# Kernel optimization log

Hardware: AMD Instinct MI355X
Metric: run time of the kernel (lower is better)

## Reference

```python
import jax, jax.numpy as jnp
import numpy as np

IMG = 1024.0
MAXD = 8.0
EPS = 1e-6
ENC_HEADS = 12
DEC_HEADS = 16


def _ln(x, w, b):
    m = jnp.mean(x, -1, keepdims=True)
    v = jnp.mean((x - m) ** 2, -1, keepdims=True)
    return (x - m) / jnp.sqrt(v + EPS) * w + b


def _attn(x, qkv_w, qkv_b, pr_w, pr_b, nh, key_mask):
    B, L, D = x.shape
    hd = D // nh
    qkv = (x @ qkv_w + qkv_b).reshape(B, L, 3, nh, hd).transpose(2, 0, 3, 1, 4)
    q, k, v = qkv[0], qkv[1], qkv[2]  # [B, nh, L, hd]
    s = jnp.einsum('bhqd,bhkd->bhqk', q, k) * (hd ** -0.5)
    if key_mask is not None:
        # restrict attention to visible tokens; identical math to per-sample gather+encode
        s = jnp.where(key_mask[:, None, None, :], s, -1e9)
    a = jax.nn.softmax(s, -1)
    o = jnp.einsum('bhqk,bhkd->bhqd', a, v).transpose(0, 2, 1, 3).reshape(B, L, D)
    return o @ pr_w + pr_b


def _block(x, i, ln1w, ln1b, qkvw, qkvb, prw, prb, ln2w, ln2b, f1w, f1b, f2w, f2b, nh, key_mask):
    x = x + _attn(_ln(x, ln1w[i], ln1b[i]), qkvw[i], qkvb[i], prw[i], prb[i], nh, key_mask)
    h = jax.nn.gelu(_ln(x, ln2w[i], ln2b[i]) @ f1w[i] + f1b[i], approximate=False)
    return x + h @ f2w[i] + f2b[i]


def _pos(coords, depths, w1, b1, w2, b2):
    x1, x2, y1, y2 = coords[..., 0], coords[..., 1], coords[..., 2], coords[..., 3]
    f = jnp.stack([(x1 + x2) / 2.0 / IMG, (y1 + y2) / 2.0 / IMG,
                   (x2 - x1) / IMG, (y2 - y1) / IMG, depths / MAXD], -1)
    return jax.nn.gelu(f @ w1 + b1, approximate=False) @ w2 + b2


def _forward(patches, coords, depths, pe_w, pe_b, pos1_w, pos1_b, pos2_w, pos2_b,
             e_ln1_w, e_ln1_b, e_qkv_w, e_qkv_b, e_pr_w, e_pr_b, e_ln2_w, e_ln2_b,
             e_f1_w, e_f1_b, e_f2_w, e_f2_b, enorm_w, enorm_b,
             de_w, de_b, mask_token, dpos1_w, dpos1_b, dpos2_w, dpos2_b,
             d_ln1_w, d_ln1_b, d_qkv_w, d_qkv_b, d_pr_w, d_pr_b, d_ln2_w, d_ln2_b,
             d_f1_w, d_f1_b, d_f2_w, d_f2_b, dnorm_w, dnorm_b,
             hi_w, hi_b, hn_w, hn_b, mask):
    B, L = mask.shape
    x = patches.reshape(B, L, -1) @ pe_w + pe_b + _pos(coords, depths, pos1_w, pos1_b, pos2_w, pos2_b)
    visible = (mask == 0)
    h = x
    for i in range(e_qkv_w.shape[0]):
        h = _block(h, i, e_ln1_w, e_ln1_b, e_qkv_w, e_qkv_b, e_pr_w, e_pr_b,
                   e_ln2_w, e_ln2_b, e_f1_w, e_f1_b, e_f2_w, e_f2_b, ENC_HEADS, visible)
    encoded = jnp.where(visible[..., None], _ln(h, enorm_w, enorm_b), 0.0)
    xd = encoded @ de_w + de_b
    xd = jnp.where((mask != 0)[..., None], mask_token, xd)
    xd = xd + _pos(coords, depths, dpos1_w, dpos1_b, dpos2_w, dpos2_b)
    for i in range(d_qkv_w.shape[0]):
        xd = _block(xd, i, d_ln1_w, d_ln1_b, d_qkv_w, d_qkv_b, d_pr_w, d_pr_b,
                    d_ln2_w, d_ln2_b, d_f1_w, d_f1_b, d_f2_w, d_f2_b, DEC_HEADS, None)
    xd = _ln(xd, dnorm_w, dnorm_b)
    return (xd @ hi_w + hi_b, xd @ hn_w + hn_b)


def setup_inputs() -> dict:
    key = jax.random.key(0)
    ks = iter(jax.random.split(key, 80))
    def nrm(shape, std=0.02):
        return jax.random.normal(next(ks), shape, jnp.float32) * std
    B, L, P, C = 4, 512, 32, 1
    D, DD = 768, 512
    ED, DDEP = 12, 8
    pd = C * P * P
    inp = {}
    inp['patches'] = jax.random.normal(next(ks), (B, L, C, P, P), jnp.float32)
    inp['coords'] = jax.random.uniform(next(ks), (B, L, 4), jnp.float32)
    inp['depths'] = jax.random.uniform(next(ks), (B, L), jnp.float32)
    inp['mask'] = jax.random.randint(next(ks), (B, L), 0, 2, jnp.int32)
    inp['pe_w'] = nrm((pd, D)); inp['pe_b'] = jnp.zeros((D,))
    inp['pos1_w'] = nrm((5, D // 2)); inp['pos1_b'] = jnp.zeros((D // 2,))
    inp['pos2_w'] = nrm((D // 2, D)); inp['pos2_b'] = jnp.zeros((D,))
    inp['e_ln1_w'] = jnp.ones((ED, D)); inp['e_ln1_b'] = jnp.zeros((ED, D))
    inp['e_qkv_w'] = nrm((ED, D, 3 * D)); inp['e_qkv_b'] = jnp.zeros((ED, 3 * D))
    inp['e_pr_w'] = nrm((ED, D, D)); inp['e_pr_b'] = jnp.zeros((ED, D))
    inp['e_ln2_w'] = jnp.ones((ED, D)); inp['e_ln2_b'] = jnp.zeros((ED, D))
    inp['e_f1_w'] = nrm((ED, D, 4 * D)); inp['e_f1_b'] = jnp.zeros((ED, 4 * D))
    inp['e_f2_w'] = nrm((ED, 4 * D, D)); inp['e_f2_b'] = jnp.zeros((ED, D))
    inp['enorm_w'] = jnp.ones((D,)); inp['enorm_b'] = jnp.zeros((D,))
    inp['de_w'] = nrm((D, DD)); inp['de_b'] = jnp.zeros((DD,))
    inp['mask_token'] = nrm((DD,))
    inp['dpos1_w'] = nrm((5, DD // 2)); inp['dpos1_b'] = jnp.zeros((DD // 2,))
    inp['dpos2_w'] = nrm((DD // 2, DD)); inp['dpos2_b'] = jnp.zeros((DD,))
    inp['d_ln1_w'] = jnp.ones((DDEP, DD)); inp['d_ln1_b'] = jnp.zeros((DDEP, DD))
    inp['d_qkv_w'] = nrm((DDEP, DD, 3 * DD)); inp['d_qkv_b'] = jnp.zeros((DDEP, 3 * DD))
    inp['d_pr_w'] = nrm((DDEP, DD, DD)); inp['d_pr_b'] = jnp.zeros((DDEP, DD))
    inp['d_ln2_w'] = jnp.ones((DDEP, DD)); inp['d_ln2_b'] = jnp.zeros((DDEP, DD))
    inp['d_f1_w'] = nrm((DDEP, DD, 4 * DD)); inp['d_f1_b'] = jnp.zeros((DDEP, 4 * DD))
    inp['d_f2_w'] = nrm((DDEP, 4 * DD, DD)); inp['d_f2_b'] = jnp.zeros((DDEP, DD))
    inp['dnorm_w'] = jnp.ones((DD,)); inp['dnorm_b'] = jnp.zeros((DD,))
    inp['hi_w'] = nrm((DD, pd)); inp['hi_b'] = jnp.zeros((pd,))
    inp['hn_w'] = nrm((DD, pd)); inp['hn_b'] = jnp.zeros((pd,))
    return inp


def reference(patches, coords, depths, pe_w, pe_b, pos1_w, pos1_b, pos2_w, pos2_b,
              e_ln1_w, e_ln1_b, e_qkv_w, e_qkv_b, e_pr_w, e_pr_b, e_ln2_w, e_ln2_b,
              e_f1_w, e_f1_b, e_f2_w, e_f2_b, enorm_w, enorm_b,
              de_w, de_b, mask_token, dpos1_w, dpos1_b, dpos2_w, dpos2_b,
              d_ln1_w, d_ln1_b, d_qkv_w, d_qkv_b, d_pr_w, d_pr_b, d_ln2_w, d_ln2_b,
              d_f1_w, d_f1_b, d_f2_w, d_f2_b, dnorm_w, dnorm_b,
              hi_w, hi_b, hn_w, hn_b, mask):
    return _forward(patches, coords, depths, pe_w, pe_b, pos1_w, pos1_b, pos2_w, pos2_b,
                    e_ln1_w, e_ln1_b, e_qkv_w, e_qkv_b, e_pr_w, e_pr_b, e_ln2_w, e_ln2_b,
                    e_f1_w, e_f1_b, e_f2_w, e_f2_b, enorm_w, enorm_b,
                    de_w, de_b, mask_token, dpos1_w, dpos1_b, dpos2_w, dpos2_b,
                    d_ln1_w, d_ln1_b, d_qkv_w, d_qkv_b, d_pr_w, d_pr_b, d_ln2_w, d_ln2_b,
                    d_f1_w, d_f1_b, d_f2_w, d_f2_b, dnorm_w, dnorm_b,
                    hi_w, hi_b, hn_w, hn_b, mask)
```

## Files before the change

kernel.cpp:

```cpp
#include <hip/hip_runtime.h>
#include <hip/hip_bf16.h>

using bf16 = __hip_bfloat16;
typedef __bf16 bf16x8 __attribute__((ext_vector_type(8)));
typedef float f32x4 __attribute__((ext_vector_type(4)));

__device__ __forceinline__ float gelu_exact(float x) {
    return 0.5f * x * (1.0f + erff(x * 0.70710678118654752440f));
}

#define GLD_LDS16(g, l) __builtin_amdgcn_global_load_lds( \
    (__attribute__((address_space(1))) void*)(g),          \
    (__attribute__((address_space(3))) void*)(l), 16, 0, 0)

template<int BM,int BN,int WM,int WN,int FM,int FN,int OUT_BF16,int HAS_BIAS,int HAS_RES,int DO_GELU>
__global__ __launch_bounds__(256, 4) void gemm_bt(
    const bf16* __restrict__ A, long lda,
    const bf16* __restrict__ Bt, long ldb,
    void* __restrict__ Cv, long ldc,
    const float* __restrict__ bias, const float* __restrict__ Res,
    int K, float alpha)
{
    static_assert(WM * WN == 4 && BM == WM * FM * 16 && BN == WN * FN * 16, "cfg");
    __shared__ alignas(16) unsigned short As[2][BM * 32];
    __shared__ alignas(16) unsigned short Bs[2][BN * 32];

    const int nwg = gridDim.x * gridDim.y;
    const int orig = blockIdx.y * gridDim.x + blockIdx.x;
    const int q = nwg >> 3, r = nwg & 7;
    const int xcd = orig & 7, seq = orig >> 3;
    const int wg = (xcd < r ? xcd * (q + 1) : r * (q + 1) + (xcd - r) * q) + seq;
    const int bn0 = (wg % gridDim.x) * BN;
    const int bm0 = (wg / gridDim.x) * BM;

    const int tid = threadIdx.x;
    const int wave = tid >> 6, lane = tid & 63;
    const int wm = (wave / WN) * (FM * 16);
    const int wn = (wave % WN) * (FN * 16);

    f32x4 acc[FM][FN] = {};

    constexpr int CA = BM / 16, CT = (BM + BN) / 16;
    constexpr int LPT = CT / 4;
    static_assert(CT % 4 == 0 && (LPT == 2 || LPT == 3), "stage cfg");
    const int lrow = lane >> 2;
    const int lcol = (((lane & 3) ^ ((lrow >> 1) & 3)) * 8);
    const int nk = K >> 5;

    const int fr = lane & 15;
    const int kg = lane >> 4;
    const int kswz = (kg ^ ((fr >> 1) & 3)) * 8;

    auto stage = [&](int buf, int kt) {
        const int k0 = kt * 32;
        for (int c = wave; c < CT; c += 4) {
            if (c < CA) {
                const bf16* src = A + (long)(bm0 + c * 16 + lrow) * lda + k0 + lcol;
                GLD_LDS16(src, &As[buf][c * 512]);
            } else {
                const int c2 = c - CA;
                const bf16* src = Bt + (long)(bn0 + c2 * 16 + lrow) * ldb + k0 + lcol;
                GLD_LDS16(src, &Bs[buf][c2 * 512]);
            }
        }
    };

    stage(0, 0);
    if (nk > 1) stage(1, 1);
    int cur = 0;
    for (int kt = 0; kt < nk; ++kt) {
        if (kt + 1 < nk) {
            if constexpr (LPT == 3) asm volatile("s_waitcnt vmcnt(3)" ::: "memory");
            else                    asm volatile("s_waitcnt vmcnt(2)" ::: "memory");
        } else {
            asm volatile("s_waitcnt vmcnt(0)" ::: "memory");
        }
        __builtin_amdgcn_s_barrier();
        __builtin_amdgcn_sched_barrier(0);

        bf16x8 af[FM], bfv[FN];
        #pragma unroll
        for (int m = 0; m < FM; ++m)
            af[m] = *(const bf16x8*)&As[cur][(wm + m * 16 + fr) * 32 + kswz];
        #pragma unroll
        for (int n = 0; n < FN; ++n)
            bfv[n] = *(const bf16x8*)&Bs[cur][(wn + n * 16 + fr) * 32 + kswz];
        #pragma unroll
        for (int m = 0; m < FM; ++m)
            #pragma unroll
            for (int n = 0; n < FN; ++n)
                acc[m][n] = __builtin_amdgcn_mfma_f32_16x16x32_bf16(af[m], bfv[n], acc[m][n], 0, 0, 0);

        __builtin_amdgcn_sched_barrier(0);
        asm volatile("s_waitcnt lgkmcnt(0)" ::: "memory");
        __builtin_amdgcn_s_barrier();
        if (kt + 2 < nk) stage(cur, kt + 2);
        cur ^= 1;
    }

    const int r0 = (lane >> 4) * 4;
    #pragma unroll
    for (int m = 0; m < FM; ++m) {
        const int rowb = bm0 + wm + m * 16 + r0;
        #pragma unroll
        for (int n = 0; n < FN; ++n) {
            const int col = bn0 + wn + n * 16 + fr;
            #pragma unroll
            for (int j = 0; j < 4; ++j) {
                float v = acc[m][n][j] * alpha;
                if (HAS_BIAS) v += bias[col];
                if (HAS_RES)  v += Res[(long)(rowb + j) * ldc + col];
                if (DO_GELU)  v = gelu_exact(v);
                const long idx = (long)(rowb + j) * ldc + col;
                if (OUT_BF16) ((bf16*)Cv)[idx] = __float2bfloat16(v);
                else          ((float*)Cv)[idx] = v;
            }
        }
    }
}

#define GEMM_A(OB,HB,HR,DG) gemm_bt<64,128,2,2,2,4, OB,HB,HR,DG>
#define GEMM_B(OB,HB,HR,DG) gemm_bt<64,64,2,2,2,2, OB,HB,HR,DG>

template<int HD, int MASKED>
__global__ __launch_bounds__(256) void flash_attn(
    const bf16* __restrict__ qkv, int ldq, int Doff, int nh,
    const bf16* __restrict__ Vt,
    bf16* __restrict__ Out, int ldo,
    const int* __restrict__ mask, float alpha)
{
    constexpr int KVT = 256, KS = HD + 8, SV = KVT + 8;
    __shared__ unsigned short Ks[KVT * KS];
    __shared__ unsigned short Vs[HD * SV];
    __shared__ unsigned short Pl[4][16 * 40];

    const int bh = blockIdx.y, b = bh / nh, h = bh % nh;
    const int tid = threadIdx.x;
    const int wave = tid >> 6, lane = tid & 63;
    const int q0 = blockIdx.x * 64 + wave * 16;
    const int fr = lane & 15, kg = lane >> 4;

    const bf16* Qb = qkv + ((long)(b * 512 + q0 + fr)) * ldq + h * HD;
    bf16x8 af[HD / 32];
    #pragma unroll
    for (int kc = 0; kc < HD / 32; ++kc)
        af[kc] = *(const bf16x8*)(Qb + kc * 32 + kg * 8);

    const bf16* Kg = qkv + (long)b * 512 * ldq + Doff + h * HD;
    const bf16* Vg = Vt + (long)bh * HD * 512;
    const int* mg = mask + (long)b * 512;

    float m[4], l[4];
    f32x4 O[HD / 16] = {};
    #pragma unroll
    for (int j = 0; j < 4; ++j) { m[j] = -INFINITY; l[j] = 0.f; }

    for (int t = 0; t < 512; t += KVT) {
        __syncthreads();
        for (int i = tid; i < KVT * (HD / 8); i += 256) {
            const int rr = i / (HD / 8), c = i % (HD / 8);
            *(bf16x8*)&Ks[rr * KS + c * 8] = *(const bf16x8*)(Kg + (long)(t + rr) * ldq + c * 8);
        }
        for (int i = tid; i < HD * (KVT / 8); i += 256) {
            const int d = i / (KVT / 8), c = i % (KVT / 8);
            *(bf16x8*)&Vs[d * SV + c * 8] = *(const bf16x8*)(Vg + (long)d * 512 + t + c * 8);
        }
        __syncthreads();

        for (int n0 = 0; n0 < KVT; n0 += 32) {
            f32x4 s[2];
            int msk[2] = {0, 0};
            #pragma unroll
            for (int f = 0; f < 2; ++f) {
                f32x4 a = {};
                #pragma unroll
                for (int kc = 0; kc < HD / 32; ++kc) {
                    bf16x8 kb = *(const bf16x8*)&Ks[(n0 + f * 16 + fr) * KS + kc * 32 + kg * 8];
                    a = __builtin_amdgcn_mfma_f32_16x16x32_bf16(af[kc], kb, a, 0, 0, 0);
                }
                #pragma unroll
                for (int j = 0; j < 4; ++j) a[j] *= alpha;
                s[f] = a;
                if (MASKED) msk[f] = mg[t + n0 + f * 16 + fr];
            }
            float g[4], p0[4], p1[4];
            #pragma unroll
            for (int j = 0; j < 4; ++j) {
                float t4 = fmaxf(s[0][j], s[1][j]);
                t4 = fmaxf(t4, __shfl_xor(t4, 1));
                t4 = fmaxf(t4, __shfl_xor(t4, 2));
                t4 = fmaxf(t4, __shfl_xor(t4, 4));
                t4 = fmaxf(t4, __shfl_xor(t4, 8));
                const float mn = fmaxf(m[j], t4);
                g[j] = __expf(m[j] - mn);
                p0[j] = msk[0] ? 0.f : __expf(s[0][j] - mn);
                p1[j] = msk[1] ? 0.f : __expf(s[1][j] - mn);
                float rs = p0[j] + p1[j];
                rs += __shfl_xor(rs, 1);
                rs += __shfl_xor(rs, 2);
                rs += __shfl_xor(rs, 4);
                rs += __shfl_xor(rs, 8);
                l[j] = l[j] * g[j] + rs;
                m[j] = mn;
            }
            #pragma unroll
            for (int dt = 0; dt < HD / 16; ++dt)
                #pragma unroll
                for (int j = 0; j < 4; ++j) O[dt][j] *= g[j];
            unsigned short* pl = &Pl[wave][0];
            #pragma unroll
            for (int j = 0; j < 4; ++j) {
                bf16 b0 = __float2bfloat16(p0[j]);
                bf16 b1 = __float2bfloat16(p1[j]);
                pl[(kg * 4 + j) * 40 + fr]      = *(unsigned short*)&b0;
                pl[(kg * 4 + j) * 40 + 16 + fr] = *(unsigned short*)&b1;
            }
            __builtin_amdgcn_sched_barrier(0);
            bf16x8 pa = *(const bf16x8*)&pl[fr * 40 + kg * 8];
            #pragma unroll
            for (int dt = 0; dt < HD / 16; ++dt) {
                bf16x8 vb = *(const bf16x8*)&Vs[(dt * 16 + fr) * SV + n0 + kg * 8];
                O[dt] = __builtin_amdgcn_mfma_f32_16x16x32_bf16(pa, vb, O[dt], 0, 0, 0);
            }
        }
    }

    float inv[4];
    #pragma unroll
    for (int j = 0; j < 4; ++j) inv[j] = 1.0f / l[j];
    #pragma unroll
    for (int dt = 0; dt < HD / 16; ++dt)
        #pragma unroll
        for (int j = 0; j < 4; ++j) {
            const long row = (long)b * 512 + q0 + kg * 4 + j;
            Out[row * ldo + h * HD + dt * 16 + fr] = __float2bfloat16(O[dt][j] * inv[j]);
        }
}

__global__ void transpose_cast_b(const float* __restrict__ in, bf16* __restrict__ out,
                                 int K, int N, int Kpad, long inS, long outS)
{
    __shared__ float tile[32][33];
    in  += (long)blockIdx.z * inS;
    out += (long)blockIdx.z * outS;
    const int n0 = blockIdx.x * 32, k0 = blockIdx.y * 32;
    const int tx = threadIdx.x & 31, ty = threadIdx.x >> 5;
    #pragma unroll
    for (int r = 0; r < 4; ++r) {
        const int k = k0 + ty + r * 8, n = n0 + tx;
        tile[ty + r * 8][tx] = (k < K && n < N) ? in[(long)k * N + n] : 0.0f;
    }
    __syncthreads();
    #pragma unroll
    for (int r = 0; r < 4; ++r) {
        const int n = n0 + ty + r * 8, k = k0 + tx;
        if (n < N && k < Kpad)
            out[(long)n * Kpad + k] = __float2bfloat16(tile[tx][ty + r * 8]);
    }
}

template<int MASKED>
__global__ void ln_kernel(const float* __restrict__ X, int Dd,
                          const float* __restrict__ w, const float* __restrict__ b,
                          bf16* __restrict__ Y, const int* __restrict__ mask)
{
    const int t = blockIdx.x, tid = threadIdx.x;
    const float* x = X + (long)t * Dd;
    float s = 0.f, s2 = 0.f;
    for (int c = tid; c < Dd; c += 256) { float v = x[c]; s += v; s2 += v * v; }
    __shared__ float sa[256], sb[256];
    sa[tid] = s; sb[tid] = s2; __syncthreads();
    for (int st = 128; st > 0; st >>= 1) {
        if (tid < st) { sa[tid] += sa[tid + st]; sb[tid] += sb[tid + st]; }
        __syncthreads();
    }
    const float mean = sa[0] / Dd;
    const float var = sb[0] / Dd - mean * mean;
    const float inv = 1.0f / sqrtf(var + 1e-6f);
    const bool zero = MASKED && (mask[t] != 0);
    for (int c = tid; c < Dd; c += 256) {
        float v = zero ? 0.0f : ((x[c] - mean) * inv * w[c] + b[c]);
        Y[(long)t * Dd + c] = __float2bfloat16(v);
    }
}

__global__ void repack_v(const unsigned short* __restrict__ qkv, int ldq, int Doff, int nh, int hd,
                         unsigned short* __restrict__ Vt)
{
    __shared__ unsigned short tile[32][33];
    const int bh = blockIdx.z, b = bh / nh, h = bh % nh;
    const int l0 = blockIdx.x * 32, d0 = blockIdx.y * 32;
    const int tx = threadIdx.x & 31, ty = threadIdx.x >> 5;
    const unsigned short* src = qkv + (long)b * 512 * ldq + 2 * Doff + h * hd;
    #pragma unroll
    for (int r = 0; r < 4; ++r)
        tile[ty + r * 8][tx] = src[(long)(l0 + ty + r * 8) * ldq + d0 + tx];
    __syncthreads();
    unsigned short* dst = Vt + (long)bh * hd * 512;
    #pragma unroll
    for (int r = 0; r < 4; ++r)
        dst[(long)(d0 + ty + r * 8) * 512 + l0 + tx] = tile[tx][ty + r * 8];
}

__global__ void build_feat(const float* __restrict__ coords, const float* __restrict__ depths,
                           bf16* __restrict__ F)
{
    const int t = blockIdx.x * 256 + threadIdx.x;
    if (t >= 2048) return;
    const float* c = coords + t * 4;
    float f[5];
    f[0] = (c[0] + c[1]) * 0.5f / 1024.0f;
    f[1] = (c[2] + c[3]) * 0.5f / 1024.0f;
    f[2] = (c[1] - c[0]) / 1024.0f;
    f[3] = (c[3] - c[2]) / 1024.0f;
    f[4] = depths[t] / 8.0f;
    bf16* o = F + (long)t * 32;
    #pragma unroll
    for (int j = 0; j < 32; ++j)
        o[j] = __float2bfloat16(j < 5 ? f[j] : 0.0f);
}

__global__ void conv_patches(const float* __restrict__ in, bf16* __restrict__ out, int n)
{
    const int i = blockIdx.x * 256 + threadIdx.x;
    if (i < n) out[i] = __float2bfloat16(in[i]);
}

__global__ void mask_pos_add(float* __restrict__ xd, const float* __restrict__ posD,
                             const int* __restrict__ mask, const float* __restrict__ token)
{
    const int i = blockIdx.x * 256 + threadIdx.x;
    const int t = i >> 9, c = i & 511;
    const float v = (mask[t] != 0) ? token[c] : xd[i];
    xd[i] = v + posD[i];
}

extern "C" void kernel_launch(void* const* d_in, const int* in_sizes, int n_in,
                              void* d_out, int out_size, void* d_ws, size_t ws_size,
                              hipStream_t stream)
{
    (void)in_sizes; (void)n_in; (void)out_size;
    const int T = 2048, D = 768, DD = 512;

    const float* patches    = (const float*)d_in[0];
    const float* coords     = (const float*)d_in[1];
    const float* depths     = (const float*)d_in[2];
    const int*   mask       = (const int*)d_in[3];
    const float* pe_w       = (const float*)d_in[4];
    const float* pe_b       = (const float*)d_in[5];
    const float* pos1_w     = (const float*)d_in[6];
    const float* pos1_b     = (const float*)d_in[7];
    const float* pos2_w     = (const float*)d_in[8];
    const float* pos2_b     = (const float*)d_in[9];
    const float* e_ln1_w    = (const float*)d_in[10];
    const float* e_ln1_b    = (const float*)d_in[11];
    const float* e_qkv_w    = (const float*)d_in[12];
    const float* e_qkv_b    = (const float*)d_in[13];
    const float* e_pr_w     = (const float*)d_in[14];
    const float* e_pr_b     = (const float*)d_in[15];
    const float* e_ln2_w    = (const float*)d_in[16];
    const float* e_ln2_b    = (const float*)d_in[17];
    const float* e_f1_w     = (const float*)d_in[18];
    const float* e_f1_b     = (const float*)d_in[19];
    const float* e_f2_w     = (const float*)d_in[20];
    const float* e_f2_b     = (const float*)d_in[21];
    const float* enorm_w    = (const float*)d_in[22];
    const float* enorm_b    = (const float*)d_in[23];
    const float* de_w       = (const float*)d_in[24];
    const float* de_b       = (const float*)d_in[25];
    const float* mask_token = (const float*)d_in[26];
    const float* dpos1_w    = (const float*)d_in[27];
    const float* dpos1_b    = (const float*)d_in[28];
    const float* dpos2_w    = (const float*)d_in[29];
    const float* dpos2_b    = (const float*)d_in[30];
    const float* d_ln1_w    = (const float*)d_in[31];
    const float* d_ln1_b    = (const float*)d_in[32];
    const float* d_qkv_w    = (const float*)d_in[33];
    const float* d_qkv_b    = (const float*)d_in[34];
    const float* d_pr_w     = (const float*)d_in[35];
    const float* d_pr_b     = (const float*)d_in[36];
    const float* d_ln2_w    = (const float*)d_in[37];
    const float* d_ln2_b    = (const float*)d_in[38];
    const float* d_f1_w     = (const float*)d_in[39];
    const float* d_f1_b     = (const float*)d_in[40];
    const float* d_f2_w     = (const float*)d_in[41];
    const float* d_f2_b     = (const float*)d_in[42];
    const float* dnorm_w    = (const float*)d_in[43];
    const float* dnorm_b    = (const float*)d_in[44];
    const float* hi_w       = (const float*)d_in[45];
    const float* hi_b       = (const float*)d_in[46];
    const float* hn_w       = (const float*)d_in[47];
    const float* hn_b       = (const float*)d_in[48];

    char* p = (char*)d_ws;
    auto alloc = [&](size_t bytes) -> char* {
        char* r = p; p += (bytes + 255) & ~(size_t)255; return r;
    };
    bf16* pe_wt  = (bf16*)alloc(768L * 1024 * 2);
    bf16* pos1t  = (bf16*)alloc(384L * 32 * 2);
    bf16* pos2t  = (bf16*)alloc(768L * 384 * 2);
    bf16* dpos1t = (bf16*)alloc(256L * 32 * 2);
    bf16* dpos2t = (bf16*)alloc(512L * 256 * 2);
    bf16* de_t   = (bf16*)alloc(512L * 768 * 2);
    bf16* hi_t   = (bf16*)alloc(1024L * 512 * 2);
    bf16* hn_t   = (bf16*)alloc(1024L * 512 * 2);
    bf16* wslot  = (bf16*)alloc(3072L * 768 * 2);
    bf16*  feat    = (bf16*)alloc(2048L * 32 * 2);
    bf16*  patchbf = (bf16*)alloc(2048L * 1024 * 2);
    bf16*  poshE   = (bf16*)alloc(2048L * 384 * 2);
    float* posE    = (float*)alloc(2048L * 768 * 4);
    bf16*  poshD   = (bf16*)alloc(2048L * 256 * 2);
    float* posD    = (float*)alloc(2048L * 512 * 4);
    float* xbuf    = (float*)alloc(2048L * 768 * 4);
    bf16*  lnbuf   = (bf16*)alloc(2048L * 768 * 2);
    bf16*  qkvbuf  = (bf16*)alloc(2048L * 2304 * 2);
    bf16*  hid     = (bf16*)alloc(2048L * 3072 * 2);
    bf16*  Vt      = (bf16*)alloc(48L * 64 * 512 * 2);
    bf16*  pin     = (bf16*)alloc(2048L * 768 * 2);
    float* xd      = (float*)alloc(2048L * 512 * 4);

    const size_t bigBytes =
        (12L*2304*768 + 12L*768*768 + 12L*3072*768 + 12L*768*3072 +
          8L*1536*512 +  8L*512*512 +  8L*2048*512 +  8L*512*2048) * 2 + 8 * 256;
    const size_t used = (size_t)(p - (char*)d_ws);
    const bool batched = ws_size >= used + bigBytes;
    bf16 *eqkvt = nullptr, *eprt = nullptr, *ef1t = nullptr, *ef2t = nullptr;
    bf16 *dqkvt = nullptr, *dprt = nullptr, *df1t = nullptr, *df2t = nullptr;
    if (batched) {
        eqkvt = (bf16*)alloc(12L * 2304 * 768 * 2);
        eprt  = (bf16*)alloc(12L * 768 * 768 * 2);
        ef1t  = (bf16*)alloc(12L * 3072 * 768 * 2);
        ef2t  = (bf16*)alloc(12L * 768 * 3072 * 2);
        dqkvt = (bf16*)alloc(8L * 1536 * 512 * 2);
        dprt  = (bf16*)alloc(8L * 512 * 512 * 2);
        df1t  = (bf16*)alloc(8L * 2048 * 512 * 2);
        df2t  = (bf16*)alloc(8L * 512 * 2048 * 2);
    }

    conv_patches<<<8192, 256, 0, stream>>>(patches, patchbf, 2097152);
    build_feat<<<8, 256, 0, stream>>>(coords, depths, feat);

    auto trb = [&](const float* in, bf16* out, int K, int N, int Kpad, int z) {
        dim3 g((N + 31) / 32, (Kpad + 31) / 32, z);
        transpose_cast_b<<<g, 256, 0, stream>>>(in, out, K, N, Kpad, (long)K * N, (long)N * Kpad);
    };
    trb(pe_w,    pe_wt,  1024,  768, 1024, 1);
    trb(pos1_w,  pos1t,     5,  384,   32, 1);
    trb(pos2_w,  pos2t,   384,  768,  384, 1);
    trb(dpos1_w, dpos1t,    5,  256,   32, 1);
    trb(dpos2_w, dpos2t,  256,  512,  256, 1);
    trb(de_w,    de_t,    768,  512,  768, 1);
    trb(hi_w,    hi_t,    512, 1024,  512, 1);
    trb(hn_w,    hn_t,    512, 1024,  512, 1);
    if (batched) {
        trb(e_qkv_w, eqkvt, 768, 2304, 768, 12);
        trb(e_pr_w,  eprt,  768,  768, 768, 12);
        trb(e_f1_w,  ef1t,  768, 3072, 768, 12);
        trb(e_f2_w,  ef2t, 3072,  768, 3072, 12);
        trb(d_qkv_w, dqkvt, 512, 1536, 512, 8);
        trb(d_pr_w,  dprt,  512,  512, 512, 8);
        trb(d_f1_w,  df1t,  512, 2048, 512, 8);
        trb(d_f2_w,  df2t, 2048,  512, 2048, 8);
    }
    auto wsl = [&](const float* src, long off, int K, int N, int Kpad) -> const bf16* {
        dim3 g((N + 31) / 32, (Kpad + 31) / 32, 1);
        transpose_cast_b<<<g, 256, 0, stream>>>(src + off, wslot, K, N, Kpad, 0, 0);
        return wslot;
    };

    GEMM_B(1,1,0,1)<<<dim3(6,32,1),256,0,stream>>>(
        feat, 32, pos1t, 32, poshE, 384, pos1_b, nullptr, 32, 1.0f);
    GEMM_B(0,1,0,0)<<<dim3(12,32,1),256,0,stream>>>(
        poshE, 384, pos2t, 384, posE, 768, pos2_b, nullptr, 384, 1.0f);
    GEMM_B(1,1,0,1)<<<dim3(4,32,1),256,0,stream>>>(
        feat, 32, dpos1t, 32, poshD, 256, dpos1_b, nullptr, 32, 1.0f);
    GEMM_B(0,1,0,0)<<<dim3(8,32,1),256,0,stream>>>(
        poshD, 256, dpos2t, 256, posD, 512, dpos2_b, nullptr, 256, 1.0f);

    GEMM_B(0,1,1,0)<<<dim3(12,32,1),256,0,stream>>>(
        patchbf, 1024, pe_wt, 1024, xbuf, 768, pe_b, posE, 1024, 1.0f);

    for (int i = 0; i < 12; ++i) {
        ln_kernel<0><<<T,256,0,stream>>>(xbuf, D, e_ln1_w + i*D, e_ln1_b + i*D, lnbuf, nullptr);
        const bf16* Wq = batched ? eqkvt + (long)i*2304*768
                                 : wsl(e_qkv_w, (long)i*768*2304, 768, 2304, 768);
        GEMM_A(1,1,0,0)<<<dim3(18,32,1),256,0,stream>>>(
            lnbuf, 768, Wq, 768, qkvbuf, 2304, e_qkv_b + i*2304, nullptr, 768, 1.0f);
        repack_v<<<dim3(16,2,48),256,0,stream>>>(
            (const unsigned short*)qkvbuf, 2304, 768, 12, 64, (unsigned short*)Vt);
        flash_attn<64,1><<<dim3(8,48),256,0,stream>>>(
            qkvbuf, 2304, 768, 12, Vt, pin, 768, mask, 0.125f);
        const bf16* Wp = batched ? eprt + (long)i*768*768
                                 : wsl(e_pr_w, (long)i*768*768, 768, 768, 768);
        GEMM_B(0,1,1,0)<<<dim3(12,32,1),256,0,stream>>>(
            pin, 768, Wp, 768, xbuf, 768, e_pr_b + i*768, xbuf, 768, 1.0f);
        ln_kernel<0><<<T,256,0,stream>>>(xbuf, D, e_ln2_w + i*D, e_ln2_b + i*D, lnbuf, nullptr);
        const bf16* W1 = batched ? ef1t + (long)i*3072*768
                                 : wsl(e_f1_w, (long)i*768*3072, 768, 3072, 768);
        GEMM_A(1,1,0,1)<<<dim3(24,32,1),256,0,stream>>>(
            lnbuf, 768, W1, 768, hid, 3072, e_f1_b + i*3072, nullptr, 768, 1.0f);
        const bf16* W2 = batched ? ef2t + (long)i*768*3072
                                 : wsl(e_f2_w, (long)i*3072*768, 3072, 768, 3072);
        GEMM_B(0,1,1,0)<<<dim3(12,32,1),256,0,stream>>>(
            hid, 3072, W2, 3072, xbuf, 768, e_f2_b + i*768, xbuf, 3072, 1.0f);
    }

    ln_kernel<1><<<T,256,0,stream>>>(xbuf, D, enorm_w, enorm_b, lnbuf, mask);
    GEMM_B(0,1,0,0)<<<dim3(8,32,1),256,0,stream>>>(
        lnbuf, 768, de_t, 768, xd, 512, de_b, nullptr, 768, 1.0f);
    mask_pos_add<<<4096,256,0,stream>>>(xd, posD, mask, mask_token);

    for (int i = 0; i < 8; ++i) {
        ln_kernel<0><<<T,256,0,stream>>>(xd, DD, d_ln1_w + i*DD, d_ln1_b + i*DD, lnbuf, nullptr);
        const bf16* Wq = batched ? dqkvt + (long)i*1536*512
                                 : wsl(d_qkv_w, (long)i*512*1536, 512, 1536, 512);
        GEMM_A(1,1,0,0)<<<dim3(12,32,1),256,0,stream>>>(
            lnbuf, 512, Wq, 512, qkvbuf, 1536, d_qkv_b + i*1536, nullptr, 512, 1.0f);
        repack_v<<<dim3(16,1,64),256,0,stream>>>(
            (const unsigned short*)qkvbuf, 1536, 512, 16, 32, (unsigned short*)Vt);
        flash_attn<32,0><<<dim3(8,64),256,0,stream>>>(
            qkvbuf, 1536, 512, 16, Vt, pin, 512, nullptr, 0.17677669529663687f);
        const bf16* Wp = batched ? dprt + (long)i*512*512
                                 : wsl(d_pr_w, (long)i*512*512, 512, 512, 512);
        GEMM_B(0,1,1,0)<<<dim3(8,32,1),256,0,stream>>>(
            pin, 512, Wp, 512, xd, 512, d_pr_b + i*512, xd, 512, 1.0f);
        ln_kernel<0><<<T,256,0,stream>>>(xd, DD, d_ln2_w + i*DD, d_ln2_b + i*DD, lnbuf, nullptr);
        const bf16* W1 = batched ? df1t + (long)i*2048*512
                                 : wsl(d_f1_w, (long)i*512*2048, 512, 2048, 512);
        GEMM_A(1,1,0,1)<<<dim3(16,32,1),256,0,stream>>>(
            lnbuf, 512, W1, 512, hid, 2048, d_f1_b + i*2048, nullptr, 512, 1.0f);
        const bf16* W2 = batched ? df2t + (long)i*512*2048
                                 : wsl(d_f2_w, (long)i*2048*512, 2048, 512, 2048);
        GEMM_B(0,1,1,0)<<<dim3(8,32,1),256,0,stream>>>(
            hid, 2048, W2, 2048, xd, 512, d_f2_b + i*512, xd, 2048, 1.0f);
    }

    ln_kernel<0><<<T,256,0,stream>>>(xd, DD, dnorm_w, dnorm_b, lnbuf, nullptr);
    float* outp = (float*)d_out;
    GEMM_B(0,1,0,0)<<<dim3(16,32,1),256,0,stream>>>(
        lnbuf, 512, hi_t, 512, outp, 1024, hi_b, nullptr, 512, 1.0f);
    GEMM_B(0,1,0,0)<<<dim3(16,32,1),256,0,stream>>>(
        lnbuf, 512, hn_t, 512, outp + 2097152, 1024, hn_b, nullptr, 512, 1.0f);
}
```

Measured before the change: 2.947 ms.

## Deepen GEMM LDS pipeline to four stages and use wave-per-row LayerNorm

```diff
diff --git a/kernel.cpp b/kernel.cpp
--- a/kernel.cpp
+++ b/kernel.cpp
@@ -12,6 +12,8 @@
 #define GLD_LDS16(g, l) __builtin_amdgcn_global_load_lds( \
     (__attribute__((address_space(1))) void*)(g),          \
     (__attribute__((address_space(3))) void*)(l), 16, 0, 0)
+
+#define WAITV(n) asm volatile("s_waitcnt vmcnt(" #n ")" ::: "memory")
 
 template<int BM,int BN,int WM,int WN,int FM,int FN,int OUT_BF16,int HAS_BIAS,int HAS_RES,int DO_GELU>
 __global__ __launch_bounds__(256, 4) void gemm_bt(
@@ -22,8 +24,8 @@
     int K, float alpha)
 {
     static_assert(WM * WN == 4 && BM == WM * FM * 16 && BN == WN * FN * 16, "cfg");
-    __shared__ alignas(16) unsigned short As[2][BM * 32];
-    __shared__ alignas(16) unsigned short Bs[2][BN * 32];
+    __shared__ alignas(16) unsigned short As[4][BM * 32];
+    __shared__ alignas(16) unsigned short Bs[4][BN * 32];
 
     const int nwg = gridDim.x * gridDim.y;
     const int orig = blockIdx.y * gridDim.x + blockIdx.x;
@@ -65,15 +67,17 @@
         }
     };
 
-    stage(0, 0);
-    if (nk > 1) stage(1, 1);
-    int cur = 0;
+    for (int i = 0; i < 4 && i < nk; ++i) stage(i, i);
+
     for (int kt = 0; kt < nk; ++kt) {
-        if (kt + 1 < nk) {
-            if constexpr (LPT == 3) asm volatile("s_waitcnt vmcnt(3)" ::: "memory");
-            else                    asm volatile("s_waitcnt vmcnt(2)" ::: "memory");
+        const int cur = kt & 3;
+        int r3 = nk - 1 - kt; if (r3 > 3) r3 = 3;
+        if constexpr (LPT == 2) {
+            switch (r3) { case 3: WAITV(6); break; case 2: WAITV(4); break;
+                          case 1: WAITV(2); break; default: WAITV(0); }
         } else {
-            asm volatile("s_waitcnt vmcnt(0)" ::: "memory");
+            switch (r3) { case 3: WAITV(9); break; case 2: WAITV(6); break;
+                          case 1: WAITV(3); break; default: WAITV(0); }
         }
         __builtin_amdgcn_s_barrier();
         __builtin_amdgcn_sched_barrier(0);
@@ -94,8 +98,7 @@
         __builtin_amdgcn_sched_barrier(0);
         asm volatile("s_waitcnt lgkmcnt(0)" ::: "memory");
         __builtin_amdgcn_s_barrier();
-        if (kt + 2 < nk) stage(cur, kt + 2);
-        cur ^= 1;
+        if (kt + 4 < nk) stage(cur, kt + 4);
     }
 
     const int r0 = (lane >> 4) * 4;
@@ -259,28 +262,33 @@
     }
 }
 
-template<int MASKED>
-__global__ void ln_kernel(const float* __restrict__ X, int Dd,
-                          const float* __restrict__ w, const float* __restrict__ b,
-                          bf16* __restrict__ Y, const int* __restrict__ mask)
-{
-    const int t = blockIdx.x, tid = threadIdx.x;
+template<int Dd, int MASKED>
+__global__ __launch_bounds__(256) void ln_wave(
+    const float* __restrict__ X, const float* __restrict__ w, const float* __restrict__ b,
+    bf16* __restrict__ Y, const int* __restrict__ mask)
+{
+    const int wave = threadIdx.x >> 6, lane = threadIdx.x & 63;
+    const int t = blockIdx.x * 4 + wave;
     const float* x = X + (long)t * Dd;
+    constexpr int NE = Dd / 64;
+    float v[NE];
     float s = 0.f, s2 = 0.f;
-    for (int c = tid; c < Dd; c += 256) { float v = x[c]; s += v; s2 += v * v; }
-    __shared__ float sa[256], sb[256];
-    sa[tid] = s; sb[tid] = s2; __syncthreads();
-    for (int st = 128; st > 0; st >>= 1) {
-        if (tid < st) { sa[tid] += sa[tid + st]; sb[tid] += sb[tid + st]; }
-        __syncthreads();
-    }
-    const float mean = sa[0] / Dd;
-    const float var = sb[0] / Dd - mean * mean;
+    #pragma unroll
+    for (int k = 0; k < NE; ++k) {
+        v[k] = x[lane + k * 64];
+        s += v[k]; s2 += v[k] * v[k];
+    }
+    #pragma unroll
+    for (int o = 32; o; o >>= 1) { s += __shfl_xor(s, o); s2 += __shfl_xor(s2, o); }
+    const float mean = s / Dd;
+    const float var = s2 / Dd - mean * mean;
     const float inv = 1.0f / sqrtf(var + 1e-6f);
     const bool zero = MASKED && (mask[t] != 0);
-    for (int c = tid; c < Dd; c += 256) {
-        float v = zero ? 0.0f : ((x[c] - mean) * inv * w[c] + b[c]);
-        Y[(long)t * Dd + c] = __float2bfloat16(v);
+    #pragma unroll
+    for (int k = 0; k < NE; ++k) {
+        const int c = lane + k * 64;
+        const float rr = zero ? 0.0f : ((v[k] - mean) * inv * w[c] + b[c]);
+        Y[(long)t * Dd + c] = __float2bfloat16(rr);
     }
 }
 
@@ -340,7 +348,7 @@
                               hipStream_t stream)
 {
     (void)in_sizes; (void)n_in; (void)out_size;
-    const int T = 2048, D = 768, DD = 512;
+    const int D = 768, DD = 512;
 
     const float* patches    = (const float*)d_in[0];
     const float* coords     = (const float*)d_in[1];
@@ -481,7 +489,7 @@
         patchbf, 1024, pe_wt, 1024, xbuf, 768, pe_b, posE, 1024, 1.0f);
 
     for (int i = 0; i < 12; ++i) {
-        ln_kernel<0><<<T,256,0,stream>>>(xbuf, D, e_ln1_w + i*D, e_ln1_b + i*D, lnbuf, nullptr);
+        ln_wave<768,0><<<512,256,0,stream>>>(xbuf, e_ln1_w + i*D, e_ln1_b + i*D, lnbuf, nullptr);
         const bf16* Wq = batched ? eqkvt + (long)i*2304*768
                                  : wsl(e_qkv_w, (long)i*768*2304, 768, 2304, 768);
         GEMM_A(1,1,0,0)<<<dim3(18,32,1),256,0,stream>>>(
@@ -494,7 +502,7 @@
                                  : wsl(e_pr_w, (long)i*768*768, 768, 768, 768);
         GEMM_B(0,1,1,0)<<<dim3(12,32,1),256,0,stream>>>(
             pin, 768, Wp, 768, xbuf, 768, e_pr_b + i*768, xbuf, 768, 1.0f);
-        ln_kernel<0><<<T,256,0,stream>>>(xbuf, D, e_ln2_w + i*D, e_ln2_b + i*D, lnbuf, nullptr);
+        ln_wave<768,0><<<512,256,0,stream>>>(xbuf, e_ln2_w + i*D, e_ln2_b + i*D, lnbuf, nullptr);
         const bf16* W1 = batched ? ef1t + (long)i*3072*768
                                  : wsl(e_f1_w, (long)i*768*3072, 768, 3072, 768);
         GEMM_A(1,1,0,1)<<<dim3(24,32,1),256,0,stream>>>(
@@ -505,13 +513,13 @@
             hid, 3072, W2, 3072, xbuf, 768, e_f2_b + i*768, xbuf, 3072, 1.0f);
     }
 
-    ln_kernel<1><<<T,256,0,stream>>>(xbuf, D, enorm_w, enorm_b, lnbuf, mask);
+    ln_wave<768,1><<<512,256,0,stream>>>(xbuf, enorm_w, enorm_b, lnbuf, mask);
     GEMM_B(0,1,0,0)<<<dim3(8,32,1),256,0,stream>>>(
         lnbuf, 768, de_t, 768, xd, 512, de_b, nullptr, 768, 1.0f);
     mask_pos_add<<<4096,256,0,stream>>>(xd, posD, mask, mask_token);
 
     for (int i = 0; i < 8; ++i) {
-        ln_kernel<0><<<T,256,0,stream>>>(xd, DD, d_ln1_w + i*DD, d_ln1_b + i*DD, lnbuf, nullptr);
+        ln_wave<512,0><<<512,256,0,stream>>>(xd, d_ln1_w + i*DD, d_ln1_b + i*DD, lnbuf, nullptr);
         const bf16* Wq = batched ? dqkvt + (long)i*1536*512
                                  : wsl(d_qkv_w, (long)i*512*1536, 512, 1536, 512);
         GEMM_A(1,1,0,0)<<<dim3(12,32,1),256,0,stream>>>(
@@ -524,7 +532,7 @@
                                  : wsl(d_pr_w, (long)i*512*512, 512, 512, 512);
         GEMM_B(0,1,1,0)<<<dim3(8,32,1),256,0,stream>>>(
             pin, 512, Wp, 512, xd, 512, d_pr_b + i*512, xd, 512, 1.0f);
-        ln_kernel<0><<<T,256,0,stream>>>(xd, DD, d_ln2_w + i*DD, d_ln2_b + i*DD, lnbuf, nullptr);
+        ln_wave<512,0><<<512,256,0,stream>>>(xd, d_ln2_w + i*DD, d_ln2_b + i*DD, lnbuf, nullptr);
         const bf16* W1 = batched ? df1t + (long)i*2048*512
                                  : wsl(d_f1_w, (long)i*512*2048, 512, 2048, 512);
         GEMM_A(1,1,0,1)<<<dim3(16,32,1),256,0,stream>>>(
@@ -535,7 +543,7 @@
             hid, 2048, W2, 2048, xd, 512, d_f2_b + i*512, xd, 2048, 1.0f);
     }
 
-    ln_kernel<0><<<T,256,0,stream>>>(xd, DD, dnorm_w, dnorm_b, lnbuf, nullptr);
+    ln_wave<512,0><<<512,256,0,stream>>>(xd, dnorm_w, dnorm_b, lnbuf, nullptr);
     float* outp = (float*)d_out;
     GEMM_B(0,1,0,0)<<<dim3(16,32,1),256,0,stream>>>(
         lnbuf, 512, hi_t, 512, outp, 1024, hi_b, nullptr, 512, 1.0f);
```

After: 2.922 ms. Within noise of the previous version (-0.9%).
